# Optimization experiments

Hardware: AMD Instinct MI355X
Metric: run time of the kernel (lower is better)

Reference implementation:

```python
import jax, jax.numpy as jnp
import numpy as np

B, D = 4096, 512
INIT_TEMP = 0.07
TEMP_MAX = 100.0


def setup_inputs() -> dict:
    key = jax.random.key(0)
    k1, k2, k3, k4 = jax.random.split(key, 4)
    return {
        "v_mean": jax.random.normal(k1, (B, D), dtype=jnp.float32),
        "v_var": jax.random.uniform(k2, (B, D), dtype=jnp.float32),
        "t_mean": jax.random.normal(k3, (B, D), dtype=jnp.float32),
        "t_var": jax.random.uniform(k4, (B, D), dtype=jnp.float32),
        "log_temp": jnp.log(jnp.asarray(1.0 / INIT_TEMP, dtype=jnp.float32)),
    }


def _pairwise_sq_dist(a, b):
    # ||a_i - b_j||^2 = ||a_i||^2 + ||b_j||^2 - 2 a_i . b_j  (GEMM expansion)
    a_sq = jnp.sum(a * a, axis=-1)            # [B]
    b_sq = jnp.sum(b * b, axis=-1)            # [B]
    cross = jnp.einsum('id,jd->ij', a, b)     # [B, B] GEMM
    return a_sq[:, None] + b_sq[None, :] - 2.0 * cross


def reference(v_mean, v_var, t_mean, t_var, log_temp):
    temperature = jnp.minimum(jnp.exp(log_temp), TEMP_MAX)
    v_sigma = jnp.sqrt(v_var)
    t_sigma = jnp.sqrt(t_var)
    # W2^2 between diagonal Gaussians (as in source: term1 + term2 only)
    w2 = _pairwise_sq_dist(v_mean, t_mean) + _pairwise_sq_dist(v_sigma, t_sigma)
    logits = -w2 * temperature                # [B, B]
    n = logits.shape[0]
    diag = jnp.arange(n)
    # CE(logits, arange): rows for image->text, columns for text->image
    logp_i = jax.nn.log_softmax(logits, axis=1)
    logp_t = jax.nn.log_softmax(logits, axis=0)
    loss_i = -jnp.mean(logp_i[diag, diag])
    loss_t = -jnp.mean(logp_t[diag, diag])
    return (loss_i + loss_t) * 0.5
```

## Files before the change

### kernel.cpp

```cpp
#include <hip/hip_runtime.h>
#include <math.h>

#define NB 4096
#define ND 512
#define K2 1024
#define NT 16

typedef __attribute__((ext_vector_type(8))) short bf16x8;
typedef __attribute__((ext_vector_type(4))) float f32x4;

__device__ __forceinline__ float wave_sum(float v) {
#pragma unroll
  for (int o = 32; o > 0; o >>= 1) v += __shfl_xor(v, o);
  return v;
}

__device__ __forceinline__ unsigned short f2bf(float x) {
  union { float f; unsigned int u; } c; c.f = x;
  unsigned int u = c.u;
  return (unsigned short)((u + 0x7fffu + ((u >> 16) & 1u)) >> 16);
}

__global__ __launch_bounds__(256) void prep_kernel(
    const float* __restrict__ v_mean, const float* __restrict__ v_var,
    const float* __restrict__ t_mean, const float* __restrict__ t_var,
    unsigned short* __restrict__ Abf, unsigned short* __restrict__ Bbf,
    float* __restrict__ a_sq, float* __restrict__ b_sq) {
  int b = blockIdx.x;
  int side = b >> 12;
  int row = b & (NB - 1);
  const float* mean = side ? t_mean : v_mean;
  const float* var = side ? t_var : v_var;
  unsigned short* dst = side ? Bbf : Abf;
  float* sq = side ? b_sq : a_sq;
  int t = threadIdx.x;
  float2 m2 = *(const float2*)(mean + (size_t)row * ND + 2 * t);
  float2 v2 = *(const float2*)(var + (size_t)row * ND + 2 * t);
  float s0 = sqrtf(v2.x), s1 = sqrtf(v2.y);
  ushort2 pm; pm.x = f2bf(m2.x); pm.y = f2bf(m2.y);
  ushort2 ps; ps.x = f2bf(s0); ps.y = f2bf(s1);
  *(ushort2*)(dst + (size_t)row * K2 + 2 * t) = pm;
  *(ushort2*)(dst + (size_t)row * K2 + ND + 2 * t) = ps;
  float p = m2.x * m2.x + m2.y * m2.y + v2.x + v2.y;
  p = wave_sum(p);
  __shared__ float sm[4];
  if ((t & 63) == 0) sm[t >> 6] = p;
  __syncthreads();
  if (t == 0) sq[row] = (sm[0] + sm[1]) + (sm[2] + sm[3]);
}

__device__ __forceinline__ void stage_tile(const unsigned short* __restrict__ G,
                                           int grow0, int k0,
                                           unsigned short* lbuf, int tid) {
#pragma unroll
  for (int s = 0; s < 4; ++s) {
    int r = s * 64 + (tid >> 3);
    int q = (tid & 7) * 16;
    int src_b = q ^ ((r & 7) << 4);
    const unsigned short* ga = G + (size_t)(grow0 + r) * K2 + k0 + (src_b >> 1);
    __builtin_amdgcn_global_load_lds(
        (const __attribute__((address_space(1))) unsigned int*)ga,
        (__attribute__((address_space(3))) unsigned int*)((char*)lbuf + s * 8192 + tid * 16),
        16, 0, 0);
  }
}

__device__ __forceinline__ bf16x8 lds_frag(const unsigned short* buf, int row, int kb) {
  return *(const bf16x8*)((const char*)buf + row * 128 + (kb ^ ((row & 7) << 4)));
}

__global__ __launch_bounds__(512) void gemm_fused_kernel(
    const unsigned short* __restrict__ Abf, const unsigned short* __restrict__ Bbf,
    const float* __restrict__ a_sq, const float* __restrict__ b_sq,
    const float* __restrict__ log_temp,
    float* __restrict__ rowM, float* __restrict__ rowS,
    float* __restrict__ colM, float* __restrict__ colS,
    float* __restrict__ diag) {
  __shared__ unsigned short ldsA[2][256 * 64];
  __shared__ unsigned short ldsB[2][256 * 64];
  int bid = blockIdx.x;
  int swz = (bid & 7) * 32 + (bid >> 3);
  int bm = swz >> 4, bn = swz & 15;
  int brow = bm * 256, bcol = bn * 256;
  int tid = threadIdx.x;
  int lane = tid & 63, wid = tid >> 6;
  int wr = wid >> 2, wc = wid & 3;
  int lr = lane & 15, lk = lane >> 4;

  f32x4 acc[8][4] = {};

  stage_tile(Abf, brow, 0, ldsA[0], tid);
  stage_tile(Bbf, bcol, 0, ldsB[0], tid);
  stage_tile(Abf, brow, 64, ldsA[1], tid);
  stage_tile(Bbf, bcol, 64, ldsB[1], tid);
  asm volatile("s_waitcnt vmcnt(8)" ::: "memory");
  __builtin_amdgcn_s_barrier();

  for (int t = 0; t < NT; ++t) {
    const int c = t & 1;
    const unsigned short* bufa = ldsA[c];
    const unsigned short* bufb = ldsB[c];
    bf16x8 af[4][2], bf0[2][2], bf1[2][2];
#pragma unroll
    for (int mi = 0; mi < 4; ++mi)
#pragma unroll
      for (int ks = 0; ks < 2; ++ks)
        af[mi][ks] = lds_frag(bufa, wr * 128 + mi * 16 + lr, ks * 64 + lk * 16);
#pragma unroll
    for (int ni = 0; ni < 2; ++ni)
#pragma unroll
      for (int ks = 0; ks < 2; ++ks)
        bf0[ni][ks] = lds_frag(bufb, wc * 64 + ni * 16 + lr, ks * 64 + lk * 16);
    __builtin_amdgcn_s_setprio(1);
#pragma unroll
    for (int mi = 0; mi < 4; ++mi)
#pragma unroll
      for (int ni = 0; ni < 2; ++ni)
#pragma unroll
        for (int ks = 0; ks < 2; ++ks)
          acc[mi][ni] = __builtin_amdgcn_mfma_f32_16x16x32_bf16(af[mi][ks], bf0[ni][ks], acc[mi][ni], 0, 0, 0);
    __builtin_amdgcn_s_setprio(0);
    __builtin_amdgcn_sched_barrier(0);
#pragma unroll
    for (int ni = 0; ni < 2; ++ni)
#pragma unroll
      for (int ks = 0; ks < 2; ++ks)
        bf1[ni][ks] = lds_frag(bufb, wc * 64 + 32 + ni * 16 + lr, ks * 64 + lk * 16);
    __builtin_amdgcn_s_setprio(1);
#pragma unroll
    for (int mi = 0; mi < 4; ++mi)
#pragma unroll
      for (int ni = 0; ni < 2; ++ni)
#pragma unroll
        for (int ks = 0; ks < 2; ++ks)
          acc[mi][2 + ni] = __builtin_amdgcn_mfma_f32_16x16x32_bf16(af[mi][ks], bf1[ni][ks], acc[mi][2 + ni], 0, 0, 0);
    __builtin_amdgcn_s_setprio(0);
    __builtin_amdgcn_sched_barrier(0);
#pragma unroll
    for (int mi = 0; mi < 4; ++mi)
#pragma unroll
      for (int ks = 0; ks < 2; ++ks)
        af[mi][ks] = lds_frag(bufa, wr * 128 + 64 + mi * 16 + lr, ks * 64 + lk * 16);
    __builtin_amdgcn_s_setprio(1);
#pragma unroll
    for (int mi = 0; mi < 4; ++mi)
#pragma unroll
      for (int ni = 0; ni < 2; ++ni)
#pragma unroll
        for (int ks = 0; ks < 2; ++ks)
          acc[4 + mi][ni] = __builtin_amdgcn_mfma_f32_16x16x32_bf16(af[mi][ks], bf0[ni][ks], acc[4 + mi][ni], 0, 0, 0);
    __builtin_amdgcn_s_setprio(0);
    __builtin_amdgcn_sched_barrier(0);
    asm volatile("s_waitcnt lgkmcnt(0)" ::: "memory");
    __builtin_amdgcn_sched_barrier(0);
    __builtin_amdgcn_s_barrier();
    if (t + 2 < NT) {
      stage_tile(Abf, brow, (t + 2) * 64, ldsA[c], tid);
      stage_tile(Bbf, bcol, (t + 2) * 64, ldsB[c], tid);
    }
    __builtin_amdgcn_sched_barrier(0);
    __builtin_amdgcn_s_setprio(1);
#pragma unroll
    for (int mi = 0; mi < 4; ++mi)
#pragma unroll
      for (int ni = 0; ni < 2; ++ni)
#pragma unroll
        for (int ks = 0; ks < 2; ++ks)
          acc[4 + mi][2 + ni] = __builtin_amdgcn_mfma_f32_16x16x32_bf16(af[mi][ks], bf1[ni][ks], acc[4 + mi][2 + ni], 0, 0, 0);
    __builtin_amdgcn_s_setprio(0);
    __builtin_amdgcn_sched_barrier(0);
    if (t < NT - 2) {
      asm volatile("s_waitcnt vmcnt(8)" ::: "memory");
    } else {
      asm volatile("s_waitcnt vmcnt(0)" ::: "memory");
    }
    __builtin_amdgcn_s_barrier();
  }

  float temp = fminf(expf(log_temp[0]), 100.0f);
#pragma unroll
  for (int m = 0; m < 8; ++m) {
#pragma unroll
    for (int r = 0; r < 4; ++r) {
      float asq = a_sq[brow + wr * 128 + m * 16 + lk * 4 + r];
#pragma unroll
      for (int n = 0; n < 4; ++n) {
        float bsq = b_sq[bcol + wc * 64 + n * 16 + lr];
        acc[m][n][r] = -temp * (asq + bsq - 2.0f * acc[m][n][r]);
      }
    }
  }
  if (bm == bn) {
#pragma unroll
    for (int m = 0; m < 8; ++m)
#pragma unroll
      for (int n = 0; n < 4; ++n)
#pragma unroll
        for (int r = 0; r < 4; ++r) {
          int rl = wr * 128 + m * 16 + lk * 4 + r;
          int cl = wc * 64 + n * 16 + lr;
          if (rl == cl) diag[brow + rl] = acc[m][n][r];
        }
  }
#pragma unroll
  for (int m = 0; m < 8; ++m) {
#pragma unroll
    for (int r = 0; r < 4; ++r) {
      float mx = fmaxf(fmaxf(acc[m][0][r], acc[m][1][r]),
                       fmaxf(acc[m][2][r], acc[m][3][r]));
#pragma unroll
      for (int o = 1; o < 16; o <<= 1) mx = fmaxf(mx, __shfl_xor(mx, o));
      float s = __expf(acc[m][0][r] - mx) + __expf(acc[m][1][r] - mx) +
                __expf(acc[m][2][r] - mx) + __expf(acc[m][3][r] - mx);
#pragma unroll
      for (int o = 1; o < 16; o <<= 1) s += __shfl_xor(s, o);
      if (lr == 0) {
        int row = brow + wr * 128 + m * 16 + lk * 4 + r;
        int ch = bn * 4 + wc;
        rowM[(size_t)row * 64 + ch] = mx;
        rowS[(size_t)row * 64 + ch] = s;
      }
    }
  }
#pragma unroll
  for (int n = 0; n < 4; ++n) {
    float mx = -INFINITY;
#pragma unroll
    for (int m = 0; m < 8; ++m)
#pragma unroll
      for (int r = 0; r < 4; ++r) mx = fmaxf(mx, acc[m][n][r]);
    mx = fmaxf(mx, __shfl_xor(mx, 16));
    float s = 0.f;
#pragma unroll
    for (int m = 0; m < 8; ++m)
#pragma unroll
      for (int r = 0; r < 4; ++r) s += __expf(acc[m][n][r] - mx);
    s += __shfl_xor(s, 16);
    if ((lk & 1) == 0) {
      int col = bcol + wc * 64 + n * 16 + lr;
      int ch = bm * 4 + wr * 2 + (lk >> 1);
      colM[(size_t)col * 64 + ch] = mx;
      colS[(size_t)col * 64 + ch] = s;
    }
  }
}

__global__ __launch_bounds__(256) void combine_kernel(
    const float* __restrict__ rowM, const float* __restrict__ rowS,
    const float* __restrict__ colM, const float* __restrict__ colS,
    const float* __restrict__ diag, float* __restrict__ hrow,
    float* __restrict__ hcol) {
  int b = blockIdx.x;
  int t = threadIdx.x;
  int wave = t >> 6, lane = t & 63;
  int isCol = b >> 10;
  int idx = (b & 1023) * 4 + wave;
  const float* PM = isCol ? colM : rowM;
  const float* PS = isCol ? colS : rowS;
  float M = PM[(size_t)idx * 64 + lane];
  float S = PS[(size_t)idx * 64 + lane];
#pragma unroll
  for (int o = 1; o < 64; o <<= 1) {
    float M2 = __shfl_xor(M, o), S2 = __shfl_xor(S, o);
    float nM = fmaxf(M, M2);
    S = S * __expf(M - nM) + S2 * __expf(M2 - nM);
    M = nM;
  }
  if (lane == 0) {
    float v = M + logf(S) - diag[idx];
    (isCol ? hcol : hrow)[idx] = v;
  }
}

__global__ __launch_bounds__(256) void final_kernel(
    const float* __restrict__ hrow, const float* __restrict__ hcol,
    float* __restrict__ out) {
  int t = threadIdx.x;
  double a = 0.0;
  for (int i = t; i < NB; i += 256) {
    a += 0.5 * ((double)hrow[i] + (double)hcol[i]);
  }
#pragma unroll
  for (int o = 32; o > 0; o >>= 1) a += __shfl_xor(a, o);
  __shared__ double sd[4];
  if ((t & 63) == 0) sd[t >> 6] = a;
  __syncthreads();
  if (t == 0) out[0] = (float)(((sd[0] + sd[1]) + (sd[2] + sd[3])) / (double)NB);
}

extern "C" void kernel_launch(void* const* d_in, const int* in_sizes, int n_in,
                              void* d_out, int out_size, void* d_ws, size_t ws_size,
                              hipStream_t stream) {
  const float* v_mean = (const float*)d_in[0];
  const float* v_var = (const float*)d_in[1];
  const float* t_mean = (const float*)d_in[2];
  const float* t_var = (const float*)d_in[3];
  const float* log_temp = (const float*)d_in[4];
  float* out = (float*)d_out;

  char* ws = (char*)d_ws;
  unsigned short* Abf = (unsigned short*)ws;
  unsigned short* Bbf = (unsigned short*)(ws + 8388608);
  float* rowM = (float*)(ws + 16777216);
  float* rowS = rowM + (size_t)NB * 64;
  float* colM = rowS + (size_t)NB * 64;
  float* colS = colM + (size_t)NB * 64;
  float* diag = colS + (size_t)NB * 64;
  float* hrow = diag + NB;
  float* hcol = hrow + NB;
  float* a_sq = hcol + NB;
  float* b_sq = a_sq + NB;

  prep_kernel<<<8192, 256, 0, stream>>>(v_mean, v_var, t_mean, t_var, Abf, Bbf, a_sq, b_sq);
  gemm_fused_kernel<<<256, 512, 0, stream>>>(Abf, Bbf, a_sq, b_sq, log_temp,
                                             rowM, rowS, colM, colS, diag);
  combine_kernel<<<2048, 256, 0, stream>>>(rowM, rowS, colM, colS, diag, hrow, hcol);
  final_kernel<<<1, 256, 0, stream>>>(hrow, hcol, out);
}
```

Baseline: 67.23 us.

## Split tile staging into per-region loads interleaved across four MFMA phases

Global-to-LDS staging of each K tile is split into four row regions, one for each quarter of A and B rows used by a compute phase. Each region's load is issued as soon as the phase that reads it has consumed its fragments, so loads spread across the iteration instead of arriving in one burst. The loop is unrolled by two to use static buffer indices, and barriers are added between phases. The extra barriers and the changed row mapping add synchronisation cost and complexity to the vmcnt accounting.

```diff
diff --git a/kernel.cpp b/kernel.cpp
--- a/kernel.cpp
+++ b/kernel.cpp
@@ -49,18 +49,19 @@
   if (t == 0) sq[row] = (sm[0] + sm[1]) + (sm[2] + sm[3]);
 }
 
-__device__ __forceinline__ void stage_tile(const unsigned short* __restrict__ G,
-                                           int grow0, int k0,
-                                           unsigned short* lbuf, int tid) {
-#pragma unroll
-  for (int s = 0; s < 4; ++s) {
-    int r = s * 64 + (tid >> 3);
+__device__ __forceinline__ void stage_region(const unsigned short* __restrict__ G,
+                                             int grow0, int k0, unsigned short* lbuf,
+                                             int tid, int off, int shift) {
+#pragma unroll
+  for (int s = 0; s < 2; ++s) {
+    int rid = s * 64 + (tid >> 3);
+    int row = off + (rid & ((1 << shift) - 1)) + ((rid >> shift) << (shift + 1));
     int q = (tid & 7) * 16;
-    int src_b = q ^ ((r & 7) << 4);
-    const unsigned short* ga = G + (size_t)(grow0 + r) * K2 + k0 + (src_b >> 1);
+    int src_b = q ^ ((row & 7) << 4);
+    const unsigned short* ga = G + (size_t)(grow0 + row) * K2 + k0 + (src_b >> 1);
     __builtin_amdgcn_global_load_lds(
         (const __attribute__((address_space(1))) unsigned int*)ga,
-        (__attribute__((address_space(3))) unsigned int*)((char*)lbuf + s * 8192 + tid * 16),
+        (__attribute__((address_space(3))) unsigned int*)((char*)lbuf + row * 128 + (tid & 7) * 16),
         16, 0, 0);
   }
 }
@@ -68,6 +69,35 @@
 __device__ __forceinline__ bf16x8 lds_frag(const unsigned short* buf, int row, int kb) {
   return *(const bf16x8*)((const char*)buf + row * 128 + (kb ^ ((row & 7) << 4)));
 }
+
+#define READ_A(dst, buf, mh)                                                   \
+  _Pragma("unroll") for (int mi = 0; mi < 4; ++mi)                             \
+  _Pragma("unroll") for (int ks = 0; ks < 2; ++ks)                             \
+      dst[mi][ks] = lds_frag(buf, wr * 128 + (mh) * 64 + mi * 16 + lr, ks * 64 + lk * 16);
+
+#define READ_B(dst, buf, nh)                                                   \
+  _Pragma("unroll") for (int ni = 0; ni < 2; ++ni)                             \
+  _Pragma("unroll") for (int ks = 0; ks < 2; ++ks)                             \
+      dst[ni][ks] = lds_frag(buf, wc * 64 + (nh) * 32 + ni * 16 + lr, ks * 64 + lk * 16);
+
+#define MFMA_QUAD(M0, N0, AF, BF)                                              \
+  __builtin_amdgcn_s_setprio(1);                                               \
+  _Pragma("unroll") for (int mi = 0; mi < 4; ++mi)                             \
+  _Pragma("unroll") for (int ni = 0; ni < 2; ++ni)                             \
+  _Pragma("unroll") for (int ks = 0; ks < 2; ++ks)                             \
+      acc[(M0) + mi][(N0) + ni] = __builtin_amdgcn_mfma_f32_16x16x32_bf16(     \
+          AF[mi][ks], BF[ni][ks], acc[(M0) + mi][(N0) + ni], 0, 0, 0);         \
+  __builtin_amdgcn_s_setprio(0);
+
+#define PHASE_SYNC()                                                           \
+  __builtin_amdgcn_sched_barrier(0);                                           \
+  __builtin_amdgcn_s_barrier();                                                \
+  asm volatile("s_waitcnt lgkmcnt(0)" ::: "memory");                           \
+  __builtin_amdgcn_sched_barrier(0);
+
+#define PHASE_END()                                                            \
+  __builtin_amdgcn_sched_barrier(0);                                           \
+  __builtin_amdgcn_s_barrier();
 
 __global__ __launch_bounds__(512) void gemm_fused_kernel(
     const unsigned short* __restrict__ Abf, const unsigned short* __restrict__ Bbf,
@@ -89,91 +119,73 @@
 
   f32x4 acc[8][4] = {};
 
-  stage_tile(Abf, brow, 0, ldsA[0], tid);
-  stage_tile(Bbf, bcol, 0, ldsB[0], tid);
-  stage_tile(Abf, brow, 64, ldsA[1], tid);
-  stage_tile(Bbf, bcol, 64, ldsB[1], tid);
+  stage_region(Abf, brow, 0, ldsA[0], tid, 0, 6);
+  stage_region(Bbf, bcol, 0, ldsB[0], tid, 0, 5);
+  stage_region(Bbf, bcol, 0, ldsB[0], tid, 32, 5);
+  stage_region(Abf, brow, 0, ldsA[0], tid, 64, 6);
+  stage_region(Abf, brow, 64, ldsA[1], tid, 0, 6);
+  stage_region(Bbf, bcol, 64, ldsB[1], tid, 0, 5);
+  stage_region(Bbf, bcol, 64, ldsB[1], tid, 32, 5);
+  stage_region(Abf, brow, 64, ldsA[1], tid, 64, 6);
   asm volatile("s_waitcnt vmcnt(8)" ::: "memory");
   __builtin_amdgcn_s_barrier();
 
-  for (int t = 0; t < NT; ++t) {
-    const int c = t & 1;
-    const unsigned short* bufa = ldsA[c];
-    const unsigned short* bufb = ldsB[c];
-    bf16x8 af[4][2], bf0[2][2], bf1[2][2];
-#pragma unroll
-    for (int mi = 0; mi < 4; ++mi)
-#pragma unroll
-      for (int ks = 0; ks < 2; ++ks)
-        af[mi][ks] = lds_frag(bufa, wr * 128 + mi * 16 + lr, ks * 64 + lk * 16);
-#pragma unroll
-    for (int ni = 0; ni < 2; ++ni)
-#pragma unroll
-      for (int ks = 0; ks < 2; ++ks)
-        bf0[ni][ks] = lds_frag(bufb, wc * 64 + ni * 16 + lr, ks * 64 + lk * 16);
-    __builtin_amdgcn_s_setprio(1);
-#pragma unroll
-    for (int mi = 0; mi < 4; ++mi)
-#pragma unroll
-      for (int ni = 0; ni < 2; ++ni)
-#pragma unroll
-        for (int ks = 0; ks < 2; ++ks)
-          acc[mi][ni] = __builtin_amdgcn_mfma_f32_16x16x32_bf16(af[mi][ks], bf0[ni][ks], acc[mi][ni], 0, 0, 0);
-    __builtin_amdgcn_s_setprio(0);
+  for (int I = 0; I < NT / 2; ++I) {
+    const int u = 2 * I;
+    const bool st = (u + 2) < NT;
+    const int ku2 = (u + 2) * 64, ku3 = (u + 3) * 64;
+    bf16x8 afL[4][2], afH[4][2], bfF[2][2], bfS[2][2];
+
+    READ_A(afL, ldsA[0], 0);
+    READ_B(bfF, ldsB[0], 0);
+    PHASE_SYNC();
+    MFMA_QUAD(0, 0, afL, bfF);
+    PHASE_END();
+    READ_B(bfS, ldsB[0], 1);
+    if (st) {
+      stage_region(Abf, brow, ku2, ldsA[0], tid, 0, 6);
+      stage_region(Bbf, bcol, ku2, ldsB[0], tid, 0, 5);
+    }
+    PHASE_SYNC();
+    MFMA_QUAD(0, 2, afL, bfS);
+    PHASE_END();
+    READ_A(afH, ldsA[0], 1);
+    if (st) stage_region(Bbf, bcol, ku2, ldsB[0], tid, 32, 5);
+    PHASE_SYNC();
+    MFMA_QUAD(4, 2, afH, bfS);
+    PHASE_END();
+    if (st) stage_region(Abf, brow, ku2, ldsA[0], tid, 64, 6);
+    PHASE_SYNC();
+    MFMA_QUAD(4, 0, afH, bfF);
     __builtin_amdgcn_sched_barrier(0);
-#pragma unroll
-    for (int ni = 0; ni < 2; ++ni)
-#pragma unroll
-      for (int ks = 0; ks < 2; ++ks)
-        bf1[ni][ks] = lds_frag(bufb, wc * 64 + 32 + ni * 16 + lr, ks * 64 + lk * 16);
-    __builtin_amdgcn_s_setprio(1);
-#pragma unroll
-    for (int mi = 0; mi < 4; ++mi)
-#pragma unroll
-      for (int ni = 0; ni < 2; ++ni)
-#pragma unroll
-        for (int ks = 0; ks < 2; ++ks)
-          acc[mi][2 + ni] = __builtin_amdgcn_mfma_f32_16x16x32_bf16(af[mi][ks], bf1[ni][ks], acc[mi][2 + ni], 0, 0, 0);
-    __builtin_amdgcn_s_setprio(0);
+    if (st) { asm volatile("s_waitcnt vmcnt(8)" ::: "memory"); }
+    else    { asm volatile("s_waitcnt vmcnt(0)" ::: "memory"); }
+    __builtin_amdgcn_s_barrier();
+
+    READ_A(afL, ldsA[1], 0);
+    READ_B(bfF, ldsB[1], 0);
+    PHASE_SYNC();
+    MFMA_QUAD(0, 0, afL, bfF);
+    PHASE_END();
+    READ_B(bfS, ldsB[1], 1);
+    if (st) {
+      stage_region(Abf, brow, ku3, ldsA[1], tid, 0, 6);
+      stage_region(Bbf, bcol, ku3, ldsB[1], tid, 0, 5);
+    }
+    PHASE_SYNC();
+    MFMA_QUAD(0, 2, afL, bfS);
+    PHASE_END();
+    READ_A(afH, ldsA[1], 1);
+    if (st) stage_region(Bbf, bcol, ku3, ldsB[1], tid, 32, 5);
+    PHASE_SYNC();
+    MFMA_QUAD(4, 2, afH, bfS);
+    PHASE_END();
+    if (st) stage_region(Abf, brow, ku3, ldsA[1], tid, 64, 6);
+    PHASE_SYNC();
+    MFMA_QUAD(4, 0, afH, bfF);
     __builtin_amdgcn_sched_barrier(0);
-#pragma unroll
-    for (int mi = 0; mi < 4; ++mi)
-#pragma unroll
-      for (int ks = 0; ks < 2; ++ks)
-        af[mi][ks] = lds_frag(bufa, wr * 128 + 64 + mi * 16 + lr, ks * 64 + lk * 16);
-    __builtin_amdgcn_s_setprio(1);
-#pragma unroll
-    for (int mi = 0; mi < 4; ++mi)
-#pragma unroll
-      for (int ni = 0; ni < 2; ++ni)
-#pragma unroll
-        for (int ks = 0; ks < 2; ++ks)
-          acc[4 + mi][ni] = __builtin_amdgcn_mfma_f32_16x16x32_bf16(af[mi][ks], bf0[ni][ks], acc[4 + mi][ni], 0, 0, 0);
-    __builtin_amdgcn_s_setprio(0);
-    __builtin_amdgcn_sched_barrier(0);
-    asm volatile("s_waitcnt lgkmcnt(0)" ::: "memory");
-    __builtin_amdgcn_sched_barrier(0);
-    __builtin_amdgcn_s_barrier();
-    if (t + 2 < NT) {
-      stage_tile(Abf, brow, (t + 2) * 64, ldsA[c], tid);
-      stage_tile(Bbf, bcol, (t + 2) * 64, ldsB[c], tid);
-    }
-    __builtin_amdgcn_sched_barrier(0);
-    __builtin_amdgcn_s_setprio(1);
-#pragma unroll
-    for (int mi = 0; mi < 4; ++mi)
-#pragma unroll
-      for (int ni = 0; ni < 2; ++ni)
-#pragma unroll
-        for (int ks = 0; ks < 2; ++ks)
-          acc[4 + mi][2 + ni] = __builtin_amdgcn_mfma_f32_16x16x32_bf16(af[mi][ks], bf1[ni][ks], acc[4 + mi][2 + ni], 0, 0, 0);
-    __builtin_amdgcn_s_setprio(0);
-    __builtin_amdgcn_sched_barrier(0);
-    if (t < NT - 2) {
-      asm volatile("s_waitcnt vmcnt(8)" ::: "memory");
-    } else {
-      asm volatile("s_waitcnt vmcnt(0)" ::: "memory");
-    }
+    if (st) { asm volatile("s_waitcnt vmcnt(8)" ::: "memory"); }
+    else    { asm volatile("s_waitcnt vmcnt(0)" ::: "memory"); }
     __builtin_amdgcn_s_barrier();
   }
 
```

New measurement: 67.76 us. About the same (+0.8%).
